# Performance work log

Hardware: AMD Instinct MI355X
Metric: run time of the kernel (lower is better)

Reference implementation:

```python
import jax, jax.numpy as jnp
import numpy as np

M, H, D, P = 16, 32, 128, 8192
N = H * D


def setup_inputs() -> dict:
    key = jax.random.key(0)
    k1, k2, k3, k4, k5, k6 = jax.random.split(key, 6)
    X = jax.random.normal(k1, (M, N), dtype=jnp.float32)
    # small init scale keeps the module's naive (unstabilized) exp-softmax finite
    Wq = jax.random.normal(k2, (N, N), dtype=jnp.float32) * 0.02
    Wk = jax.random.normal(k3, (N, N), dtype=jnp.float32) * 0.02
    Wv = jax.random.normal(k4, (N, N), dtype=jnp.float32) * 0.02
    cache_K = jax.random.normal(k5, (H, P, D), dtype=jnp.float32) * 0.05
    cache_V = jax.random.normal(k6, (H, P, D), dtype=jnp.float32)
    return {"X": X, "Wq": Wq, "Wk": Wk, "Wv": Wv,
            "cache_K": cache_K, "cache_V": cache_V}


def reference(X, Wq, Wk, Wv, cache_K, cache_V):
    m, n = X.shape                      # [M, N]
    h, p, d = cache_K.shape             # [H, P, D]
    # RMSNorm (no learned scale, matches (X*X).sum / N)
    x2 = jnp.sum(X * X, axis=1)
    x_norm = X / jnp.sqrt(x2 / n)[:, None]
    # QKV projections (nn.Linear, no bias -> x @ W.T)
    q = (x_norm @ Wq.T).reshape(m, h, d).transpose(1, 0, 2)   # [H, M, D]
    k = (x_norm @ Wk.T).reshape(m, h, d).transpose(1, 0, 2)   # [H, M, D]
    v = (x_norm @ Wv.T).reshape(m, h, d).transpose(1, 0, 2)   # [H, M, D]
    # append to cache
    ck = jnp.concatenate([cache_K, k], axis=1)                # [H, P+M, D]
    cv = jnp.concatenate([cache_V, v], axis=1)                # [H, P+M, D]
    # scores (no 1/sqrt(D) scaling in the original) + naive softmax
    c = jnp.einsum('hmd,hpd->hmp', q, ck)                     # [H, M, P+M]
    c_exp = jnp.exp(c)
    c_div = c_exp / jnp.sum(c_exp, axis=2, keepdims=True)
    o = jnp.einsum('hmp,hpd->hmd', c_div, cv)                 # [H, M, D]
    return o.transpose(1, 0, 2).reshape(m, n)                 # [M, N]
```

## Files before the change

### kernel.cpp

```cpp
#include <hip/hip_runtime.h>

#define NN 4096
#define HH 32
#define DD 128
#define MM 16
#define PP 8192

__device__ __forceinline__ float4 ld4(const float* p) { return *(const float4*)(p); }
__device__ __forceinline__ float dot4f(float4 a, float4 b) {
  return a.x * b.x + a.y * b.y + a.z * b.z + a.w * b.w;
}

__global__ void k1_rms(const float* __restrict__ X, float* __restrict__ inv) {
  const int m = blockIdx.x;
  const int tid = threadIdx.x;
  float s = 0.f;
#pragma unroll
  for (int i = 0; i < 16; ++i) {
    float v = X[(size_t)m * NN + i * 256 + tid];
    s += v * v;
  }
#pragma unroll
  for (int off = 1; off < 64; off <<= 1) s += __shfl_xor(s, off, 64);
  __shared__ float red[4];
  if ((tid & 63) == 0) red[tid >> 6] = s;
  __syncthreads();
  if (tid == 0) {
    float t = red[0] + red[1] + red[2] + red[3];
    inv[m] = rsqrtf(t * (1.0f / (float)NN));
  }
}

__global__ __launch_bounds__(256, 3) void k2_qkv(
    const float* __restrict__ X, const float* __restrict__ Wq,
    const float* __restrict__ Wk, const float* __restrict__ Wv,
    float* __restrict__ c_part) {
  __shared__ float wt[2][4][1024];
  __shared__ float lds_c[4][32][17];
  const int b = blockIdx.x;
  const int mat = b >> 9;
  const int qt = (b >> 7) & 3;
  const int rb = b & 127;
  const float* W = (mat == 0) ? Wq : (mat == 1) ? Wk : Wv;
  const int tid = threadIdx.x;
  const int wave = tid >> 6;
  const int lane = tid & 63;
  const int m4 = lane & 3;
  const int g = lane >> 2;
  const int kwin = wave * 256 + g * 16;
  const int kbase = qt * 1024 + kwin;

  float4 xr[4][4];
#pragma unroll
  for (int mi = 0; mi < 4; ++mi) {
    const float* xp = X + (size_t)(mi * 4 + m4) * NN + kbase;
#pragma unroll
    for (int j = 0; j < 4; ++j) xr[mi][j] = ld4(xp + j * 4);
  }

  const float* Wbase = W + (size_t)(rb * 32) * NN + qt * 1024;
  float4 rw[4];
#pragma unroll
  for (int i = 0; i < 4; ++i) {
    const int id = tid + i * 256;
    rw[i] = *((const float4*)(Wbase + (size_t)(id >> 8) * NN) + (id & 255));
  }

  for (int tt = 0; tt < 8; ++tt) {
    __syncthreads();
#pragma unroll
    for (int i = 0; i < 4; ++i)
      ((float4*)wt[tt & 1])[tid + i * 256] = rw[i];
    __syncthreads();
    if (tt < 7) {
      const float* Wn = Wbase + (size_t)((tt + 1) * 4) * NN;
#pragma unroll
      for (int i = 0; i < 4; ++i) {
        const int id = tid + i * 256;
        rw[i] = *((const float4*)(Wn + (size_t)(id >> 8) * NN) + (id & 255));
      }
    }
    float acc[4][4];
#pragma unroll
    for (int r = 0; r < 4; ++r)
#pragma unroll
      for (int mi = 0; mi < 4; ++mi) acc[r][mi] = 0.f;
#pragma unroll
    for (int r = 0; r < 4; ++r) {
      const float* wp = wt[tt & 1][r] + kwin;
      float4 w0 = ld4(wp), w1 = ld4(wp + 4), w2 = ld4(wp + 8), w3 = ld4(wp + 12);
#pragma unroll
      for (int mi = 0; mi < 4; ++mi)
        acc[r][mi] += dot4f(xr[mi][0], w0) + dot4f(xr[mi][1], w1) +
                      dot4f(xr[mi][2], w2) + dot4f(xr[mi][3], w3);
    }
#pragma unroll
    for (int off = 4; off < 64; off <<= 1)
#pragma unroll
      for (int r = 0; r < 4; ++r)
#pragma unroll
        for (int mi = 0; mi < 4; ++mi)
          acc[r][mi] += __shfl_xor(acc[r][mi], off, 64);
    if (g == 0) {
#pragma unroll
      for (int r = 0; r < 4; ++r)
#pragma unroll
        for (int mi = 0; mi < 4; ++mi)
          lds_c[wave][tt * 4 + r][mi * 4 + m4] = acc[r][mi];
    }
  }
  __syncthreads();
#pragma unroll
  for (int i = 0; i < 2; ++i) {
    const int idx = i * 256 + tid;
    const int l = idx >> 4;
    const int m = idx & 15;
    float s = lds_c[0][l][m] + lds_c[1][l][m] + lds_c[2][l][m] + lds_c[3][l][m];
    c_part[(((size_t)(mat * 4 + qt) * 16 + m) << 12) + (rb * 32 + l)] = s;
  }
}

__global__ void k2b_combine(const float* __restrict__ c_part,
                            const float* __restrict__ inv,
                            float* __restrict__ qkv) {
  const int t = blockIdx.x * 256 + threadIdx.x;
  const int mat = t >> 16;
  const int r = t & 65535;
  const int m = r >> 12;
  const int j = r & 4095;
  float s = 0.f;
#pragma unroll
  for (int qt = 0; qt < 4; ++qt)
    s += c_part[(((size_t)(mat * 4 + qt) * 16 + m) << 12) + j];
  qkv[(((size_t)(mat * 16 + m)) << 12) + j] = s * inv[m];
}

__global__ __launch_bounds__(256, 4) void k3_attn(
    const float* __restrict__ cK, const float* __restrict__ cV,
    const float* __restrict__ qkv, float* __restrict__ o_part,
    float* __restrict__ den_part) {
  __shared__ float sO[4][16][132];
  __shared__ float sD[4][16];
  const int b = blockIdx.x;
  const int h = b >> 5;
  const int seg = b & 31;
  const int tid = threadIdx.x;
  const int wave = tid >> 6;
  const int lane = tid & 63;
  const int m8 = lane & 7;
  const int g = lane >> 3;
  const int d0 = g * 16;

  float4 q0[4], q1[4];
  {
    const float* qa = qkv + (size_t)m8 * NN + h * DD + d0;
    const float* qb = qkv + (size_t)(m8 + 8) * NN + h * DD + d0;
#pragma unroll
    for (int j = 0; j < 4; ++j) { q0[j] = ld4(qa + j * 4); q1[j] = ld4(qb + j * 4); }
  }
  float o0[16], o1[16];
#pragma unroll
  for (int j = 0; j < 16; ++j) { o0[j] = 0.f; o1[j] = 0.f; }
  float den0 = 0.f, den1 = 0.f;

  const size_t rowbase = (size_t)h * PP + (size_t)seg * 256 + wave * 64;
  const float* kp = cK + rowbase * DD + d0;
  const float* vp = cV + rowbase * DD + d0;

  for (int i = 0; i < 64; ++i) {
    float4 k0 = ld4(kp), k1 = ld4(kp + 4), k2 = ld4(kp + 8), k3 = ld4(kp + 12);
    float4 v0 = ld4(vp), v1 = ld4(vp + 4), v2 = ld4(vp + 8), v3 = ld4(vp + 12);
    kp += DD; vp += DD;
    float c0 = dot4f(q0[0], k0) + dot4f(q0[1], k1) + dot4f(q0[2], k2) + dot4f(q0[3], k3);
    float c1 = dot4f(q1[0], k0) + dot4f(q1[1], k1) + dot4f(q1[2], k2) + dot4f(q1[3], k3);
#pragma unroll
    for (int off = 8; off < 64; off <<= 1) {
      c0 += __shfl_xor(c0, off, 64);
      c1 += __shfl_xor(c1, off, 64);
    }
    float e0 = __expf(c0), e1 = __expf(c1);
    den0 += e0; den1 += e1;
    o0[0] += e0 * v0.x;  o0[1] += e0 * v0.y;  o0[2] += e0 * v0.z;  o0[3] += e0 * v0.w;
    o0[4] += e0 * v1.x;  o0[5] += e0 * v1.y;  o0[6] += e0 * v1.z;  o0[7] += e0 * v1.w;
    o0[8] += e0 * v2.x;  o0[9] += e0 * v2.y;  o0[10] += e0 * v2.z; o0[11] += e0 * v2.w;
    o0[12] += e0 * v3.x; o0[13] += e0 * v3.y; o0[14] += e0 * v3.z; o0[15] += e0 * v3.w;
    o1[0] += e1 * v0.x;  o1[1] += e1 * v0.y;  o1[2] += e1 * v0.z;  o1[3] += e1 * v0.w;
    o1[4] += e1 * v1.x;  o1[5] += e1 * v1.y;  o1[6] += e1 * v1.z;  o1[7] += e1 * v1.w;
    o1[8] += e1 * v2.x;  o1[9] += e1 * v2.y;  o1[10] += e1 * v2.z; o1[11] += e1 * v2.w;
    o1[12] += e1 * v3.x; o1[13] += e1 * v3.y; o1[14] += e1 * v3.z; o1[15] += e1 * v3.w;
  }

  if (seg == h) {
#pragma unroll
    for (int pi = 0; pi < 4; ++pi) {
      const int p = wave * 4 + pi;
      const float* kq = qkv + (size_t)(16 + p) * NN + h * DD + d0;
      const float* vq = qkv + (size_t)(32 + p) * NN + h * DD + d0;
      float4 k0 = ld4(kq), k1 = ld4(kq + 4), k2 = ld4(kq + 8), k3 = ld4(kq + 12);
      float c0 = dot4f(q0[0], k0) + dot4f(q0[1], k1) + dot4f(q0[2], k2) + dot4f(q0[3], k3);
      float c1 = dot4f(q1[0], k0) + dot4f(q1[1], k1) + dot4f(q1[2], k2) + dot4f(q1[3], k3);
#pragma unroll
      for (int off = 8; off < 64; off <<= 1) {
        c0 += __shfl_xor(c0, off, 64);
        c1 += __shfl_xor(c1, off, 64);
      }
      float e0 = __expf(c0), e1 = __expf(c1);
      den0 += e0; den1 += e1;
      float4 v0 = ld4(vq), v1 = ld4(vq + 4), v2 = ld4(vq + 8), v3 = ld4(vq + 12);
      o0[0] += e0 * v0.x;  o0[1] += e0 * v0.y;  o0[2] += e0 * v0.z;  o0[3] += e0 * v0.w;
      o0[4] += e0 * v1.x;  o0[5] += e0 * v1.y;  o0[6] += e0 * v1.z;  o0[7] += e0 * v1.w;
      o0[8] += e0 * v2.x;  o0[9] += e0 * v2.y;  o0[10] += e0 * v2.z; o0[11] += e0 * v2.w;
      o0[12] += e0 * v3.x; o0[13] += e0 * v3.y; o0[14] += e0 * v3.z; o0[15] += e0 * v3.w;
      o1[0] += e1 * v0.x;  o1[1] += e1 * v0.y;  o1[2] += e1 * v0.z;  o1[3] += e1 * v0.w;
      o1[4] += e1 * v1.x;  o1[5] += e1 * v1.y;  o1[6] += e1 * v1.z;  o1[7] += e1 * v1.w;
      o1[8] += e1 * v2.x;  o1[9] += e1 * v2.y;  o1[10] += e1 * v2.z; o1[11] += e1 * v2.w;
      o1[12] += e1 * v3.x; o1[13] += e1 * v3.y; o1[14] += e1 * v3.z; o1[15] += e1 * v3.w;
    }
  }

#pragma unroll
  for (int j = 0; j < 4; ++j) {
    *(float4*)&sO[wave][m8][d0 + j * 4] =
        make_float4(o0[j * 4], o0[j * 4 + 1], o0[j * 4 + 2], o0[j * 4 + 3]);
    *(float4*)&sO[wave][m8 + 8][d0 + j * 4] =
        make_float4(o1[j * 4], o1[j * 4 + 1], o1[j * 4 + 2], o1[j * 4 + 3]);
  }
  if (g == 0) { sD[wave][m8] = den0; sD[wave][8 + m8] = den1; }
  __syncthreads();
#pragma unroll
  for (int e = 0; e < 8; ++e) {
    const int idx = e * 256 + tid;
    const int m = idx >> 7;
    const int d = idx & 127;
    o_part[(size_t)b * 2048 + idx] =
        sO[0][m][d] + sO[1][m][d] + sO[2][m][d] + sO[3][m][d];
  }
  if (tid < 16)
    den_part[(size_t)b * 16 + tid] =
        sD[0][tid] + sD[1][tid] + sD[2][tid] + sD[3][tid];
}

__global__ void k4_final(const float* __restrict__ o_part,
                         const float* __restrict__ den_part,
                         float* __restrict__ out) {
  const int b = blockIdx.x;
  const int h = b >> 3;
  const int tid = threadIdx.x;
  const int idx = (b & 7) * 256 + tid;
  __shared__ float dinv[16];
  if (tid < 16) {
    float s = 0.f;
    for (int j = 0; j < 32; ++j) s += den_part[(size_t)h * 512 + j * 16 + tid];
    dinv[tid] = 1.0f / s;
  }
  __syncthreads();
  float s = 0.f;
  for (int j = 0; j < 32; ++j) s += o_part[(size_t)h * 65536 + j * 2048 + idx];
  const int m = idx >> 7;
  const int d = idx & 127;
  out[(size_t)m * NN + h * DD + d] = s * dinv[m];
}

extern "C" void kernel_launch(void* const* d_in, const int* in_sizes, int n_in,
                              void* d_out, int out_size, void* d_ws, size_t ws_size,
                              hipStream_t stream) {
  (void)in_sizes; (void)n_in; (void)out_size; (void)ws_size;
  const float* X  = (const float*)d_in[0];
  const float* Wq = (const float*)d_in[1];
  const float* Wk = (const float*)d_in[2];
  const float* Wv = (const float*)d_in[3];
  const float* cK = (const float*)d_in[4];
  const float* cV = (const float*)d_in[5];
  float* out = (float*)d_out;
  float* ws = (float*)d_ws;

  float* inv      = ws;
  float* c_part   = ws + 16;
  float* qkv      = c_part + 786432;
  float* o_part   = qkv + 196608;
  float* den_part = o_part + 2097152;

  k1_rms<<<16, 256, 0, stream>>>(X, inv);
  k2_qkv<<<1536, 256, 0, stream>>>(X, Wq, Wk, Wv, c_part);
  k2b_combine<<<768, 256, 0, stream>>>(c_part, inv, qkv);
  k3_attn<<<dim3(1024), 256, 0, stream>>>(cK, cV, qkv, o_part, den_part);
  k4_final<<<256, 256, 0, stream>>>(o_part, den_part, out);
}
```

Baseline: 479.8 us.

## Stream W rows from global into registers and prefetch K rows in attention

New measurement: 775.6 us. 61.7% more time.

```diff
diff --git a/kernel.cpp b/kernel.cpp
--- a/kernel.cpp
+++ b/kernel.cpp
@@ -31,12 +31,11 @@
   }
 }
 
-__global__ __launch_bounds__(256, 3) void k2_qkv(
+__global__ __launch_bounds__(256, 4) void k2_qkv(
     const float* __restrict__ X, const float* __restrict__ Wq,
     const float* __restrict__ Wk, const float* __restrict__ Wv,
     float* __restrict__ c_part) {
-  __shared__ float wt[2][4][1024];
-  __shared__ float lds_c[4][32][17];
+  __shared__ float lds_c[4][4][32][20];
   const int b = blockIdx.x;
   const int mat = b >> 9;
   const int qt = (b >> 7) & 3;
@@ -47,8 +46,7 @@
   const int lane = tid & 63;
   const int m4 = lane & 3;
   const int g = lane >> 2;
-  const int kwin = wave * 256 + g * 16;
-  const int kbase = qt * 1024 + kwin;
+  const int kbase = qt * 1024 + wave * 256 + g * 16;
 
   float4 xr[4][4];
 #pragma unroll
@@ -58,64 +56,48 @@
     for (int j = 0; j < 4; ++j) xr[mi][j] = ld4(xp + j * 4);
   }
 
-  const float* Wbase = W + (size_t)(rb * 32) * NN + qt * 1024;
-  float4 rw[4];
-#pragma unroll
-  for (int i = 0; i < 4; ++i) {
-    const int id = tid + i * 256;
-    rw[i] = *((const float4*)(Wbase + (size_t)(id >> 8) * NN) + (id & 255));
-  }
-
-  for (int tt = 0; tt < 8; ++tt) {
-    __syncthreads();
-#pragma unroll
-    for (int i = 0; i < 4; ++i)
-      ((float4*)wt[tt & 1])[tid + i * 256] = rw[i];
-    __syncthreads();
-    if (tt < 7) {
-      const float* Wn = Wbase + (size_t)((tt + 1) * 4) * NN;
-#pragma unroll
-      for (int i = 0; i < 4; ++i) {
-        const int id = tid + i * 256;
-        rw[i] = *((const float4*)(Wn + (size_t)(id >> 8) * NN) + (id & 255));
-      }
-    }
-    float acc[4][4];
-#pragma unroll
-    for (int r = 0; r < 4; ++r)
-#pragma unroll
-      for (int mi = 0; mi < 4; ++mi) acc[r][mi] = 0.f;
-#pragma unroll
-    for (int r = 0; r < 4; ++r) {
-      const float* wp = wt[tt & 1][r] + kwin;
-      float4 w0 = ld4(wp), w1 = ld4(wp + 4), w2 = ld4(wp + 8), w3 = ld4(wp + 12);
-#pragma unroll
-      for (int mi = 0; mi < 4; ++mi)
-        acc[r][mi] += dot4f(xr[mi][0], w0) + dot4f(xr[mi][1], w1) +
-                      dot4f(xr[mi][2], w2) + dot4f(xr[mi][3], w3);
-    }
-#pragma unroll
-    for (int off = 4; off < 64; off <<= 1)
-#pragma unroll
-      for (int r = 0; r < 4; ++r)
-#pragma unroll
-        for (int mi = 0; mi < 4; ++mi)
-          acc[r][mi] += __shfl_xor(acc[r][mi], off, 64);
-    if (g == 0) {
-#pragma unroll
-      for (int r = 0; r < 4; ++r)
-#pragma unroll
-        for (int mi = 0; mi < 4; ++mi)
-          lds_c[wave][tt * 4 + r][mi * 4 + m4] = acc[r][mi];
-    }
+  const float* Wp = W + (size_t)(rb * 32) * NN + kbase;
+  float4 wc[4], wn[4];
+#pragma unroll
+  for (int j = 0; j < 4; ++j) wc[j] = ld4(Wp + j * 4);
+  const float* Wnext = Wp + NN;
+
+#pragma unroll 2
+  for (int r = 0; r < 32; ++r) {
+    if (r < 31) {
+#pragma unroll
+      for (int j = 0; j < 4; ++j) wn[j] = ld4(Wnext + j * 4);
+      Wnext += NN;
+    }
+    float a0 = dot4f(xr[0][0], wc[0]) + dot4f(xr[0][1], wc[1]) +
+               dot4f(xr[0][2], wc[2]) + dot4f(xr[0][3], wc[3]);
+    float a1 = dot4f(xr[1][0], wc[0]) + dot4f(xr[1][1], wc[1]) +
+               dot4f(xr[1][2], wc[2]) + dot4f(xr[1][3], wc[3]);
+    float a2 = dot4f(xr[2][0], wc[0]) + dot4f(xr[2][1], wc[1]) +
+               dot4f(xr[2][2], wc[2]) + dot4f(xr[2][3], wc[3]);
+    float a3 = dot4f(xr[3][0], wc[0]) + dot4f(xr[3][1], wc[1]) +
+               dot4f(xr[3][2], wc[2]) + dot4f(xr[3][3], wc[3]);
+    a0 += __shfl_xor(a0, 16, 64); a1 += __shfl_xor(a1, 16, 64);
+    a2 += __shfl_xor(a2, 16, 64); a3 += __shfl_xor(a3, 16, 64);
+    a0 += __shfl_xor(a0, 32, 64); a1 += __shfl_xor(a1, 32, 64);
+    a2 += __shfl_xor(a2, 32, 64); a3 += __shfl_xor(a3, 32, 64);
+    if (g < 4)
+      *(float4*)&lds_c[wave][g][r][m4 * 4] = make_float4(a0, a1, a2, a3);
+#pragma unroll
+    for (int j = 0; j < 4; ++j) wc[j] = wn[j];
   }
   __syncthreads();
 #pragma unroll
   for (int i = 0; i < 2; ++i) {
-    const int idx = i * 256 + tid;
-    const int l = idx >> 4;
-    const int m = idx & 15;
-    float s = lds_c[0][l][m] + lds_c[1][l][m] + lds_c[2][l][m] + lds_c[3][l][m];
+    const int o = i * 256 + tid;
+    const int m = o >> 5;
+    const int l = o & 31;
+    const int col = (m & 3) * 4 + (m >> 2);
+    float s = 0.f;
+#pragma unroll
+    for (int w = 0; w < 4; ++w)
+#pragma unroll
+      for (int gq = 0; gq < 4; ++gq) s += lds_c[w][gq][l][col];
     c_part[(((size_t)(mat * 4 + qt) * 16 + m) << 12) + (rb * 32 + l)] = s;
   }
 }
@@ -167,12 +149,24 @@
   const float* kp = cK + rowbase * DD + d0;
   const float* vp = cV + rowbase * DD + d0;
 
+  float4 ck[4], nk[4], cv[4];
+#pragma unroll
+  for (int j = 0; j < 4; ++j) ck[j] = ld4(kp + j * 4);
+
+#pragma unroll 2
   for (int i = 0; i < 64; ++i) {
-    float4 k0 = ld4(kp), k1 = ld4(kp + 4), k2 = ld4(kp + 8), k3 = ld4(kp + 12);
-    float4 v0 = ld4(vp), v1 = ld4(vp + 4), v2 = ld4(vp + 8), v3 = ld4(vp + 12);
-    kp += DD; vp += DD;
-    float c0 = dot4f(q0[0], k0) + dot4f(q0[1], k1) + dot4f(q0[2], k2) + dot4f(q0[3], k3);
-    float c1 = dot4f(q1[0], k0) + dot4f(q1[1], k1) + dot4f(q1[2], k2) + dot4f(q1[3], k3);
+#pragma unroll
+    for (int j = 0; j < 4; ++j) cv[j] = ld4(vp + j * 4);
+    vp += DD;
+    if (i < 63) {
+      kp += DD;
+#pragma unroll
+      for (int j = 0; j < 4; ++j) nk[j] = ld4(kp + j * 4);
+    }
+    float c0 = dot4f(q0[0], ck[0]) + dot4f(q0[1], ck[1]) +
+               dot4f(q0[2], ck[2]) + dot4f(q0[3], ck[3]);
+    float c1 = dot4f(q1[0], ck[0]) + dot4f(q1[1], ck[1]) +
+               dot4f(q1[2], ck[2]) + dot4f(q1[3], ck[3]);
 #pragma unroll
     for (int off = 8; off < 64; off <<= 1) {
       c0 += __shfl_xor(c0, off, 64);
@@ -180,14 +174,16 @@
     }
     float e0 = __expf(c0), e1 = __expf(c1);
     den0 += e0; den1 += e1;
-    o0[0] += e0 * v0.x;  o0[1] += e0 * v0.y;  o0[2] += e0 * v0.z;  o0[3] += e0 * v0.w;
-    o0[4] += e0 * v1.x;  o0[5] += e0 * v1.y;  o0[6] += e0 * v1.z;  o0[7] += e0 * v1.w;
-    o0[8] += e0 * v2.x;  o0[9] += e0 * v2.y;  o0[10] += e0 * v2.z; o0[11] += e0 * v2.w;
-    o0[12] += e0 * v3.x; o0[13] += e0 * v3.y; o0[14] += e0 * v3.z; o0[15] += e0 * v3.w;
-    o1[0] += e1 * v0.x;  o1[1] += e1 * v0.y;  o1[2] += e1 * v0.z;  o1[3] += e1 * v0.w;
-    o1[4] += e1 * v1.x;  o1[5] += e1 * v1.y;  o1[6] += e1 * v1.z;  o1[7] += e1 * v1.w;
-    o1[8] += e1 * v2.x;  o1[9] += e1 * v2.y;  o1[10] += e1 * v2.z; o1[11] += e1 * v2.w;
-    o1[12] += e1 * v3.x; o1[13] += e1 * v3.y; o1[14] += e1 * v3.z; o1[15] += e1 * v3.w;
+    o0[0] += e0 * cv[0].x;  o0[1] += e0 * cv[0].y;  o0[2] += e0 * cv[0].z;  o0[3] += e0 * cv[0].w;
+    o0[4] += e0 * cv[1].x;  o0[5] += e0 * cv[1].y;  o0[6] += e0 * cv[1].z;  o0[7] += e0 * cv[1].w;
+    o0[8] += e0 * cv[2].x;  o0[9] += e0 * cv[2].y;  o0[10] += e0 * cv[2].z; o0[11] += e0 * cv[2].w;
+    o0[12] += e0 * cv[3].x; o0[13] += e0 * cv[3].y; o0[14] += e0 * cv[3].z; o0[15] += e0 * cv[3].w;
+    o1[0] += e1 * cv[0].x;  o1[1] += e1 * cv[0].y;  o1[2] += e1 * cv[0].z;  o1[3] += e1 * cv[0].w;
+    o1[4] += e1 * cv[1].x;  o1[5] += e1 * cv[1].y;  o1[6] += e1 * cv[1].z;  o1[7] += e1 * cv[1].w;
+    o1[8] += e1 * cv[2].x;  o1[9] += e1 * cv[2].y;  o1[10] += e1 * cv[2].z; o1[11] += e1 * cv[2].w;
+    o1[12] += e1 * cv[3].x; o1[13] += e1 * cv[3].y; o1[14] += e1 * cv[3].z; o1[15] += e1 * cv[3].w;
+#pragma unroll
+    for (int j = 0; j < 4; ++j) ck[j] = nk[j];
   }
 
   if (seg == h) {
```
